# Performance work log

Measured on AMD Instinct MI355X. Metric: run time of the kernel, lower is better.

The kernel has to match this reference:

```python
import jax, jax.numpy as jnp
import numpy as np

D_IN = 768
D_OUT = 768
NUM_HEADS = 12
HEAD_DIM = D_OUT // NUM_HEADS


def setup_inputs() -> dict:
    key = jax.random.key(0)
    ks = jax.random.split(key, 6)
    s = 1.0 / np.sqrt(D_IN)
    X = jax.random.normal(ks[0], (4, 2048, D_IN), dtype=jnp.float32)
    Wq = jax.random.uniform(ks[1], (D_IN, D_OUT), jnp.float32, -s, s)
    Wk = jax.random.uniform(ks[2], (D_IN, D_OUT), jnp.float32, -s, s)
    Wv = jax.random.uniform(ks[3], (D_IN, D_OUT), jnp.float32, -s, s)
    Wo = jax.random.uniform(ks[4], (D_OUT, D_OUT), jnp.float32, -s, s)
    bo = jax.random.uniform(ks[5], (D_OUT,), jnp.float32, -s, s)
    return {"X": X, "Wq": Wq, "Wk": Wk, "Wv": Wv, "Wo": Wo, "bo": bo}


def reference(X, Wq, Wk, Wv, Wo, bo):
    b, n, _ = X.shape
    # QKV projections, split heads -> [b, h, n, d]
    def split(t):
        return t.reshape(b, n, NUM_HEADS, HEAD_DIM).transpose(0, 2, 1, 3)
    q = split(X @ Wq)
    k = split(X @ Wk)
    v = split(X @ Wv)
    scores = jnp.einsum('bhqd,bhkd->bhqk', q, k) / np.sqrt(HEAD_DIM).astype(np.float32)
    causal = jnp.triu(jnp.ones((n, n), dtype=bool), k=1)
    scores = jnp.where(causal, -jnp.inf, scores)
    attn = jax.nn.softmax(scores, axis=-1)  # dropout p=0 -> identity
    ctx = jnp.einsum('bhqk,bhkd->bhqd', attn, v)
    ctx = ctx.transpose(0, 2, 1, 3).reshape(b, n, D_OUT)
    return ctx @ Wo + bo
```

## Files before the change

kernel.cpp:

```cpp
#include <hip/hip_runtime.h>
#include <stdint.h>

#define B_  4
#define N_  2048
#define D_  768
#define H_  12
#define HD_ 64
#define M_  (B_*N_)

typedef short bf8 __attribute__((ext_vector_type(8)));
typedef float f32x4 __attribute__((ext_vector_type(4)));

static __device__ __forceinline__ unsigned short f2bf(float f) {
    unsigned u = __float_as_uint(f);
    unsigned r = u + 0x7fffu + ((u >> 16) & 1u);
    return (unsigned short)(r >> 16);
}

static __device__ __forceinline__ unsigned pk2bf(float f0, float f1) {
    return ((__float_as_uint(f1) + 0x8000u) & 0xFFFF0000u) |
           ((__float_as_uint(f0) + 0x8000u) >> 16);
}

#if __has_builtin(__builtin_amdgcn_exp2f)
#define EXP2(x) __builtin_amdgcn_exp2f(x)
#else
#define EXP2(x) exp2f(x)
#endif

#define GLOAD_LDS16(gptr, lptr)                                                   \
    __builtin_amdgcn_global_load_lds(                                             \
        (const __attribute__((address_space(1))) void*)(gptr),                    \
        (__attribute__((address_space(3))) void*)(lptr), 16, 0, 0)

#define QSCALE 0.1803368801111204f

__global__ __launch_bounds__(256) void convert_x(const float* __restrict__ X,
                                                 unsigned short* __restrict__ Xb) {
    const size_t i = ((size_t)blockIdx.x * 256 + threadIdx.x) * 8;
    const float4 a = *(const float4*)(X + i);
    const float4 b = *(const float4*)(X + i + 4);
    ushort4 lo, hi;
    lo.x = f2bf(a.x); lo.y = f2bf(a.y); lo.z = f2bf(a.z); lo.w = f2bf(a.w);
    hi.x = f2bf(b.x); hi.y = f2bf(b.y); hi.z = f2bf(b.z); hi.w = f2bf(b.w);
    *(ushort4*)(Xb + i)     = lo;
    *(ushort4*)(Xb + i + 4) = hi;
}

__global__ __launch_bounds__(256) void transpose_w(
    const float* __restrict__ Wq, const float* __restrict__ Wk,
    const float* __restrict__ Wv, const float* __restrict__ Wo,
    unsigned short* __restrict__ Wqt, unsigned short* __restrict__ Wkt,
    unsigned short* __restrict__ Wvt, unsigned short* __restrict__ Wot)
{
    __shared__ float tile[32][33];
    const int z = blockIdx.z;
    const float* W = (z == 0) ? Wq : (z == 1) ? Wk : (z == 2) ? Wv : Wo;
    unsigned short* Wt = (z == 0) ? Wqt : (z == 1) ? Wkt : (z == 2) ? Wvt : Wot;
    const int k0 = blockIdx.x * 32, n0 = blockIdx.y * 32;
    const int tx = threadIdx.x & 31, ty = threadIdx.x >> 5;
    #pragma unroll
    for (int i = 0; i < 4; ++i)
        tile[ty + 8 * i][tx] = W[(size_t)(k0 + ty + 8 * i) * D_ + n0 + tx];
    __syncthreads();
    #pragma unroll
    for (int i = 0; i < 4; ++i)
        Wt[(size_t)(n0 + ty + 8 * i) * D_ + k0 + tx] = f2bf(tile[tx][ty + 8 * i]);
}

__global__ __launch_bounds__(256) void qkv_mfma(
    const unsigned short* __restrict__ Xb,
    const unsigned short* __restrict__ Wqt, const unsigned short* __restrict__ Wkt,
    const unsigned short* __restrict__ Wvt,
    unsigned short* __restrict__ Qb, unsigned short* __restrict__ Kb,
    unsigned short* __restrict__ Vt)
{
    __shared__ unsigned short As[8192];
    __shared__ unsigned short Bs[8192];

    const int t = threadIdx.x;
    const int wave = t >> 6, lane = t & 63;
    const int col = lane & 15, quad = lane >> 4;
    const int wm = (wave & 1) * 64, wn = (wave >> 1) * 64;

    const int m0 = blockIdx.x * 128;
    const int n0 = blockIdx.y * 128;
    const int mat = blockIdx.z;
    const unsigned short* Wt = (mat == 0) ? Wqt : (mat == 1) ? Wkt : Wvt;
    const bool sw = (mat != 2);

    const unsigned short* Ag = Xb + (size_t)(m0 + (t >> 2)) * D_ + (t & 3) * 8;
    const unsigned short* Bg = Wt + (size_t)(n0 + (t >> 2)) * D_ + (t & 3) * 8;
    unsigned short* AsD = As + t * 8;
    unsigned short* BsD = Bs + t * 8;

    f32x4 acc[4][4] = {};

    for (int k0 = 0; k0 < D_; k0 += 64) {
        __syncthreads();
        GLOAD_LDS16(Ag + k0,                        AsD);
        GLOAD_LDS16(Ag + k0 + 32,                   AsD + 4096);
        GLOAD_LDS16(Ag + (size_t)64 * D_ + k0,      AsD + 2048);
        GLOAD_LDS16(Ag + (size_t)64 * D_ + k0 + 32, AsD + 6144);
        GLOAD_LDS16(Bg + k0,                        BsD);
        GLOAD_LDS16(Bg + k0 + 32,                   BsD + 4096);
        GLOAD_LDS16(Bg + (size_t)64 * D_ + k0,      BsD + 2048);
        GLOAD_LDS16(Bg + (size_t)64 * D_ + k0 + 32, BsD + 6144);
        __syncthreads();

        #pragma unroll
        for (int ks = 0; ks < 2; ++ks) {
            bf8 a[4], b[4];
            #pragma unroll
            for (int i = 0; i < 4; ++i)
                a[i] = *(const bf8*)(As + ks * 4096 + (wm + i * 16 + col) * 32 + quad * 8);
            #pragma unroll
            for (int j = 0; j < 4; ++j)
                b[j] = *(const bf8*)(Bs + ks * 4096 + (wn + j * 16 + col) * 32 + quad * 8);
            if (sw) {
                #pragma unroll
                for (int i = 0; i < 4; ++i)
                    #pragma unroll
                    for (int j = 0; j < 4; ++j)
                        acc[i][j] = __builtin_amdgcn_mfma_f32_16x16x32_bf16(b[j], a[i], acc[i][j], 0, 0, 0);
            } else {
                #pragma unroll
                for (int i = 0; i < 4; ++i)
                    #pragma unroll
                    for (int j = 0; j < 4; ++j)
                        acc[i][j] = __builtin_amdgcn_mfma_f32_16x16x32_bf16(a[i], b[j], acc[i][j], 0, 0, 0);
            }
        }
    }

    if (sw) {
        unsigned short* Out = (mat == 0) ? Qb : Kb;
        const float qsc = (mat == 0) ? QSCALE : 1.0f;
        #pragma unroll
        for (int i = 0; i < 4; ++i) {
            const int token = m0 + wm + i * 16 + col;
            const int bb = token >> 11, nn = token & (N_ - 1);
            #pragma unroll
            for (int j = 0; j < 4; ++j) {
                const int n = n0 + wn + j * 16 + quad * 4;
                const int h = n >> 6, d = n & 63;
                ushort4 pk;
                pk.x = f2bf(acc[i][j][0] * qsc);
                pk.y = f2bf(acc[i][j][1] * qsc);
                pk.z = f2bf(acc[i][j][2] * qsc);
                pk.w = f2bf(acc[i][j][3] * qsc);
                *(ushort4*)(Out + ((size_t)(bb * H_ + h) * N_ + nn) * HD_ + d) = pk;
            }
        }
    } else {
        #pragma unroll
        for (int j = 0; j < 4; ++j) {
            const int n = n0 + wn + j * 16 + col;
            const int h = n >> 6, d = n & 63;
            #pragma unroll
            for (int i = 0; i < 4; ++i) {
                const int mb = m0 + wm + i * 16 + quad * 4;
                const int bb = mb >> 11;
                const int nn = mb & (N_ - 1);
                const int nnp = (nn & ~31) | ((quad >> 1) << 4) | ((quad & 1) << 3) |
                                ((i & 1) << 2);
                ushort4 pk;
                pk.x = f2bf(acc[i][j][0]); pk.y = f2bf(acc[i][j][1]);
                pk.z = f2bf(acc[i][j][2]); pk.w = f2bf(acc[i][j][3]);
                *(ushort4*)(Vt + ((size_t)(bb * H_ + h) * HD_ + d) * N_ + nnp) = pk;
            }
        }
    }
}

#define PS 72

static __device__ __forceinline__ void qk_softmax(
    const bf8 (&ka)[4][2], bf8 qb0, bf8 qb1,
    int k0, int q, bool mask, float& lpart,
    bf8& pb0, bf8& pb1, int quad)
{
    f32x4 s[4] = {};
    __builtin_amdgcn_s_setprio(1);
    #pragma unroll
    for (int kc = 0; kc < 4; ++kc) {
        s[kc] = __builtin_amdgcn_mfma_f32_16x16x32_bf16(ka[kc][0], qb0, s[kc], 0, 0, 0);
        s[kc] = __builtin_amdgcn_mfma_f32_16x16x32_bf16(ka[kc][1], qb1, s[kc], 0, 0, 0);
    }
    __builtin_amdgcn_s_setprio(0);

    float p[4][4];
    if (mask) {
        #pragma unroll
        for (int kc = 0; kc < 4; ++kc)
            #pragma unroll
            for (int r = 0; r < 4; ++r) {
                const int key = k0 + kc * 16 + quad * 4 + r;
                p[kc][r] = EXP2((key > q) ? -INFINITY : s[kc][r]);
            }
    } else {
        #pragma unroll
        for (int kc = 0; kc < 4; ++kc)
            #pragma unroll
            for (int r = 0; r < 4; ++r) p[kc][r] = EXP2(s[kc][r]);
    }

    #pragma unroll
    for (int kc = 0; kc < 4; ++kc)
        #pragma unroll
        for (int r = 0; r < 4; ++r) lpart += p[kc][r];

    uint4 u0, u1;
    u0.x = pk2bf(p[0][0], p[0][1]); u0.y = pk2bf(p[0][2], p[0][3]);
    u0.z = pk2bf(p[1][0], p[1][1]); u0.w = pk2bf(p[1][2], p[1][3]);
    u1.x = pk2bf(p[2][0], p[2][1]); u1.y = pk2bf(p[2][2], p[2][3]);
    u1.z = pk2bf(p[3][0], p[3][1]); u1.w = pk2bf(p[3][2], p[3][3]);
    pb0 = *(bf8*)&u0;
    pb1 = *(bf8*)&u1;
}

static __device__ __forceinline__ void pv_acc(
    bf8 pb0, bf8 pb1, const bf8 (&va)[4][2], f32x4 (&o)[4])
{
    __builtin_amdgcn_s_setprio(1);
    #pragma unroll
    for (int dc = 0; dc < 4; ++dc) {
        o[dc] = __builtin_amdgcn_mfma_f32_16x16x32_bf16(va[dc][0], pb0, o[dc], 0, 0, 0);
        o[dc] = __builtin_amdgcn_mfma_f32_16x16x32_bf16(va[dc][1], pb1, o[dc], 0, 0, 0);
    }
    __builtin_amdgcn_s_setprio(0);
}

__global__ __launch_bounds__(256, 3) void attn_mfma(
    const unsigned short* __restrict__ Qb,
    const unsigned short* __restrict__ Kb,
    const unsigned short* __restrict__ Vt,
    unsigned short* __restrict__ Ctxb)
{
    __shared__ unsigned short Kl[2][64 * PS];
    __shared__ unsigned short Vl[2][64 * PS];

    const int t = threadIdx.x;
    const int wave = t >> 6;
    const int lane = t & 63;
    const int col  = lane & 15;
    const int quad = lane >> 4;

    const int bid = blockIdx.x;
    const int bh  = bid >> 4;
    const int x   = bid & 15;
    const int tl  = x, th = 31 - x;
    const int q0L = tl * 64 + wave * 16;
    const int q0H = th * 64 + wave * 16;
    const int qL  = q0L + col;
    const int qH  = q0H + col;

    const unsigned short* Kp = Kb + (size_t)bh * N_ * HD_;
    const unsigned short* Vp = Vt + (size_t)bh * HD_ * N_;
    const unsigned short* QpL = Qb + ((size_t)bh * N_ + q0L) * HD_;
    const unsigned short* QpH = Qb + ((size_t)bh * N_ + q0H) * HD_;

    const bf8 qbL0 = *(const bf8*)(QpL + (size_t)col * HD_ + quad * 8);
    const bf8 qbL1 = *(const bf8*)(QpL + (size_t)col * HD_ + 32 + quad * 8);
    const bf8 qbH0 = *(const bf8*)(QpH + (size_t)col * HD_ + quad * 8);
    const bf8 qbH1 = *(const bf8*)(QpH + (size_t)col * HD_ + 32 + quad * 8);

    f32x4 oL[4] = {}, oH[4] = {};
    float lL = 0.f, lH = 0.f;

    const int srow = t >> 3;
    const int scol = (t & 7) * 8;
    const unsigned short* Kg = Kp + (size_t)srow * HD_ + scol;
    const unsigned short* Vg = Vp + (size_t)srow * N_ + scol;
    const int kO0 = srow * PS + scol;
    const int kO1 = (srow + 32) * PS + scol;

    const int iters = 32 - x;

    uint4 kr0 = *(const uint4*)(Kg);
    uint4 kr1 = *(const uint4*)(Kg + (size_t)32 * HD_);
    uint4 vr0 = *(const uint4*)(Vg);
    uint4 vr1 = *(const uint4*)(Vg + (size_t)32 * N_);
    *(uint4*)(Kl[0] + kO0) = kr0;
    *(uint4*)(Kl[0] + kO1) = kr1;
    *(uint4*)(Vl[0] + kO0) = vr0;
    *(uint4*)(Vl[0] + kO1) = vr1;
    kr0 = *(const uint4*)(Kg + (size_t)64 * HD_);
    kr1 = *(const uint4*)(Kg + (size_t)96 * HD_);
    vr0 = *(const uint4*)(Vg + 64);
    vr1 = *(const uint4*)(Vg + (size_t)32 * N_ + 64);

    for (int kt = 0; kt < iters; ++kt) {
        const int k0 = kt * 64;
        const bool actL = (kt <= tl);
        const unsigned short* Kc = Kl[kt & 1];
        const unsigned short* Vc = Vl[kt & 1];
        unsigned short* Kn = Kl[(kt + 1) & 1];
        unsigned short* Vn = Vl[(kt + 1) & 1];

        __syncthreads();

        if (kt + 1 < iters) {
            *(uint4*)(Kn + kO0) = kr0;
            *(uint4*)(Kn + kO1) = kr1;
            *(uint4*)(Vn + kO0) = vr0;
            *(uint4*)(Vn + kO1) = vr1;
        }
        if (kt + 2 < iters) {
            const size_t k2 = (size_t)(kt + 2) * 64;
            kr0 = *(const uint4*)(Kg + k2 * HD_);
            kr1 = *(const uint4*)(Kg + (k2 + 32) * HD_);
            vr0 = *(const uint4*)(Vg + k2);
            vr1 = *(const uint4*)(Vg + (size_t)32 * N_ + k2);
        }

        bf8 ka[4][2];
        #pragma unroll
        for (int kc = 0; kc < 4; ++kc) {
            ka[kc][0] = *(const bf8*)(Kc + (kc * 16 + col) * PS + quad * 8);
            ka[kc][1] = *(const bf8*)(Kc + (kc * 16 + col) * PS + 32 + quad * 8);
        }

        bf8 va[4][2];
        #pragma unroll
        for (int dc = 0; dc < 4; ++dc) {
            va[dc][0] = *(const bf8*)(Vc + (dc * 16 + col) * PS + quad * 8);
            va[dc][1] = *(const bf8*)(Vc + (dc * 16 + col) * PS + 32 + quad * 8);
        }

        bf8 pbH0, pbH1;
        qk_softmax(ka, qbH0, qbH1, k0, qH, kt == th, lH, pbH0, pbH1, quad);
        pv_acc(pbH0, pbH1, va, oH);

        if (actL) {
            bf8 pbL0, pbL1;
            qk_softmax(ka, qbL0, qbL1, k0, qL, kt == tl, lL, pbL0, pbL1, quad);
            pv_acc(pbL0, pbL1, va, oL);
        }
    }

    const int b = bh / H_;
    const int h = bh % H_;
    {
        float l = lH;
        l += __shfl_xor(l, 16, 64);
        l += __shfl_xor(l, 32, 64);
        const float inv = 1.0f / l;
        unsigned short* cp = Ctxb + ((size_t)(b * N_ + qH)) * D_ + h * HD_;
        #pragma unroll
        for (int dc = 0; dc < 4; ++dc) {
            uint2 pk;
            pk.x = pk2bf(oH[dc][0] * inv, oH[dc][1] * inv);
            pk.y = pk2bf(oH[dc][2] * inv, oH[dc][3] * inv);
            *(uint2*)(cp + dc * 16 + quad * 4) = pk;
        }
    }
    {
        float l = lL;
        l += __shfl_xor(l, 16, 64);
        l += __shfl_xor(l, 32, 64);
        const float inv = 1.0f / l;
        unsigned short* cp = Ctxb + ((size_t)(b * N_ + qL)) * D_ + h * HD_;
        #pragma unroll
        for (int dc = 0; dc < 4; ++dc) {
            uint2 pk;
            pk.x = pk2bf(oL[dc][0] * inv, oL[dc][1] * inv);
            pk.y = pk2bf(oL[dc][2] * inv, oL[dc][3] * inv);
            *(uint2*)(cp + dc * 16 + quad * 4) = pk;
        }
    }
}

__global__ __launch_bounds__(256) void out_mfma(
    const unsigned short* __restrict__ Ctxb,
    const unsigned short* __restrict__ Wot,
    const float* __restrict__ bo,
    float* __restrict__ Out)
{
    __shared__ unsigned short As[8192];
    __shared__ unsigned short Bs[8192];

    const int t = threadIdx.x;
    const int wave = t >> 6, lane = t & 63;
    const int col = lane & 15, quad = lane >> 4;
    const int wm = (wave & 1) * 64, wn = (wave >> 1) * 64;

    const int m0 = blockIdx.x * 128;
    const int n0 = blockIdx.y * 128;

    const unsigned short* Ag = Ctxb + (size_t)(m0 + (t >> 2)) * D_ + (t & 3) * 8;
    const unsigned short* Bg = Wot + (size_t)(n0 + (t >> 2)) * D_ + (t & 3) * 8;
    unsigned short* AsD = As + t * 8;
    unsigned short* BsD = Bs + t * 8;

    f32x4 acc[4][4] = {};

    for (int k0 = 0; k0 < D_; k0 += 64) {
        __syncthreads();
        GLOAD_LDS16(Ag + k0,                        AsD);
        GLOAD_LDS16(Ag + k0 + 32,                   AsD + 4096);
        GLOAD_LDS16(Ag + (size_t)64 * D_ + k0,      AsD + 2048);
        GLOAD_LDS16(Ag + (size_t)64 * D_ + k0 + 32, AsD + 6144);
        GLOAD_LDS16(Bg + k0,                        BsD);
        GLOAD_LDS16(Bg + k0 + 32,                   BsD + 4096);
        GLOAD_LDS16(Bg + (size_t)64 * D_ + k0,      BsD + 2048);
        GLOAD_LDS16(Bg + (size_t)64 * D_ + k0 + 32, BsD + 6144);
        __syncthreads();

        #pragma unroll
        for (int ks = 0; ks < 2; ++ks) {
            bf8 a[4], b[4];
            #pragma unroll
            for (int i = 0; i < 4; ++i)
                a[i] = *(const bf8*)(As + ks * 4096 + (wm + i * 16 + col) * 32 + quad * 8);
            #pragma unroll
            for (int j = 0; j < 4; ++j)
                b[j] = *(const bf8*)(Bs + ks * 4096 + (wn + j * 16 + col) * 32 + quad * 8);
            #pragma unroll
            for (int i = 0; i < 4; ++i)
                #pragma unroll
                for (int j = 0; j < 4; ++j)
                    acc[i][j] = __builtin_amdgcn_mfma_f32_16x16x32_bf16(b[j], a[i], acc[i][j], 0, 0, 0);
        }
    }

    #pragma unroll
    for (int i = 0; i < 4; ++i) {
        const int m = m0 + wm + i * 16 + col;
        #pragma unroll
        for (int j = 0; j < 4; ++j) {
            const int n = n0 + wn + j * 16 + quad * 4;
            const float4 bias = *(const float4*)(bo + n);
            float4 o;
            o.x = acc[i][j][0] + bias.x;
            o.y = acc[i][j][1] + bias.y;
            o.z = acc[i][j][2] + bias.z;
            o.w = acc[i][j][3] + bias.w;
            *(float4*)(Out + (size_t)m * D_ + n) = o;
        }
    }
}

extern "C" void kernel_launch(void* const* d_in, const int* in_sizes, int n_in,
                              void* d_out, int out_size, void* d_ws, size_t ws_size,
                              hipStream_t stream) {
    const float* X  = (const float*)d_in[0];
    const float* Wq = (const float*)d_in[1];
    const float* Wk = (const float*)d_in[2];
    const float* Wv = (const float*)d_in[3];
    const float* Wo = (const float*)d_in[4];
    const float* bo = (const float*)d_in[5];
    float* out = (float*)d_out;

    const size_t elems = (size_t)M_ * D_;
    const size_t welems = (size_t)D_ * D_;
    unsigned short* Xb  = (unsigned short*)d_ws;
    unsigned short* Wqt = Xb + elems;
    unsigned short* Wkt = Wqt + welems;
    unsigned short* Wvt = Wkt + welems;
    unsigned short* Wot = Wvt + welems;
    unsigned short* Qb  = Wot + welems;
    unsigned short* Kb  = Qb + elems;
    unsigned short* Vt  = Kb + elems;
    unsigned short* Ctxb = Xb;

    convert_x<<<dim3(elems / 2048), 256, 0, stream>>>(X, Xb);
    transpose_w<<<dim3(24, 24, 4), 256, 0, stream>>>(Wq, Wk, Wv, Wo, Wqt, Wkt, Wvt, Wot);

    qkv_mfma<<<dim3(M_ / 128, D_ / 128, 3), 256, 0, stream>>>(Xb, Wqt, Wkt, Wvt, Qb, Kb, Vt);

    attn_mfma<<<dim3(B_ * H_ * 16), 256, 0, stream>>>(Qb, Kb, Vt, Ctxb);

    out_mfma<<<dim3(M_ / 128, D_ / 128), 256, 0, stream>>>(Ctxb, Wot, bo, out);
}
```

Before: 213.1 us.

## Remap block IDs for XCD-aware L2 locality and interleave QK MFMAs

Flattens the grids of the QKV and output GEMMs into 1D and remaps block IDs so that consecutive blocks on the same XCD (id mod 8) cover neighbouring tiles that share A and W data in L2. The attention kernel gets the same remap, so the 16 query-tile pairs of one head land on one XCD and reuse K/V. The attention loop also splits the QK MFMA step from the softmax and issues both the high and low QK MFMA groups before either softmax, which gives the scheduler more independent work to overlap. This costs more live registers (two score arrays), which could hurt occupancy at launch bounds of 3.

```diff
diff --git a/kernel.cpp b/kernel.cpp
--- a/kernel.cpp
+++ b/kernel.cpp
@@ -83,9 +83,12 @@
     const int col = lane & 15, quad = lane >> 4;
     const int wm = (wave & 1) * 64, wn = (wave >> 1) * 64;
 
-    const int m0 = blockIdx.x * 128;
-    const int n0 = blockIdx.y * 128;
-    const int mat = blockIdx.z;
+    const int orig = blockIdx.x;
+    const int wgid = (orig & 7) * 144 + (orig >> 3);
+    const int m0  = (wgid / 18) * 128;
+    const int nm  = wgid % 18;
+    const int mat = nm / 6;
+    const int n0  = (nm % 6) * 128;
     const unsigned short* Wt = (mat == 0) ? Wqt : (mat == 1) ? Wkt : Wvt;
     const bool sw = (mat != 2);
 
@@ -175,12 +178,9 @@
 
 #define PS 72
 
-static __device__ __forceinline__ void qk_softmax(
-    const bf8 (&ka)[4][2], bf8 qb0, bf8 qb1,
-    int k0, int q, bool mask, float& lpart,
-    bf8& pb0, bf8& pb1, int quad)
-{
-    f32x4 s[4] = {};
+static __device__ __forceinline__ void qk_mfma8(
+    const bf8 (&ka)[4][2], bf8 qb0, bf8 qb1, f32x4 (&s)[4])
+{
     __builtin_amdgcn_s_setprio(1);
     #pragma unroll
     for (int kc = 0; kc < 4; ++kc) {
@@ -188,7 +188,12 @@
         s[kc] = __builtin_amdgcn_mfma_f32_16x16x32_bf16(ka[kc][1], qb1, s[kc], 0, 0, 0);
     }
     __builtin_amdgcn_s_setprio(0);
-
+}
+
+static __device__ __forceinline__ void softmax_pack(
+    const f32x4 (&s)[4], int k0, int q, bool mask, float& lpart,
+    bf8& pb0, bf8& pb1, int quad)
+{
     float p[4][4];
     if (mask) {
         #pragma unroll
@@ -246,7 +251,8 @@
     const int col  = lane & 15;
     const int quad = lane >> 4;
 
-    const int bid = blockIdx.x;
+    const int orig = blockIdx.x;
+    const int bid  = (orig & 7) * 96 + (orig >> 3);
     const int bh  = bid >> 4;
     const int x   = bid & 15;
     const int tl  = x, th = 31 - x;
@@ -328,13 +334,18 @@
             va[dc][1] = *(const bf8*)(Vc + (dc * 16 + col) * PS + 32 + quad * 8);
         }
 
+        f32x4 sH[4] = {};
+        qk_mfma8(ka, qbH0, qbH1, sH);
+        f32x4 sL[4] = {};
+        if (actL) qk_mfma8(ka, qbL0, qbL1, sL);
+
         bf8 pbH0, pbH1;
-        qk_softmax(ka, qbH0, qbH1, k0, qH, kt == th, lH, pbH0, pbH1, quad);
+        softmax_pack(sH, k0, qH, kt == th, lH, pbH0, pbH1, quad);
         pv_acc(pbH0, pbH1, va, oH);
 
         if (actL) {
             bf8 pbL0, pbL1;
-            qk_softmax(ka, qbL0, qbL1, k0, qL, kt == tl, lL, pbL0, pbL1, quad);
+            softmax_pack(sL, k0, qL, kt == tl, lL, pbL0, pbL1, quad);
             pv_acc(pbL0, pbL1, va, oL);
         }
     }
@@ -385,8 +396,10 @@
     const int col = lane & 15, quad = lane >> 4;
     const int wm = (wave & 1) * 64, wn = (wave >> 1) * 64;
 
-    const int m0 = blockIdx.x * 128;
-    const int n0 = blockIdx.y * 128;
+    const int orig = blockIdx.x;
+    const int wgid = (orig & 7) * 48 + (orig >> 3);
+    const int m0 = (wgid / 6) * 128;
+    const int n0 = (wgid % 6) * 128;
 
     const unsigned short* Ag = Ctxb + (size_t)(m0 + (t >> 2)) * D_ + (t & 3) * 8;
     const unsigned short* Bg = Wot + (size_t)(n0 + (t >> 2)) * D_ + (t & 3) * 8;
@@ -467,9 +480,9 @@
     convert_x<<<dim3(elems / 2048), 256, 0, stream>>>(X, Xb);
     transpose_w<<<dim3(24, 24, 4), 256, 0, stream>>>(Wq, Wk, Wv, Wo, Wqt, Wkt, Wvt, Wot);
 
-    qkv_mfma<<<dim3(M_ / 128, D_ / 128, 3), 256, 0, stream>>>(Xb, Wqt, Wkt, Wvt, Qb, Kb, Vt);
+    qkv_mfma<<<dim3(1152), 256, 0, stream>>>(Xb, Wqt, Wkt, Wvt, Qb, Kb, Vt);
 
     attn_mfma<<<dim3(B_ * H_ * 16), 256, 0, stream>>>(Qb, Kb, Vt, Ctxb);
 
-    out_mfma<<<dim3(M_ / 128, D_ / 128), 256, 0, stream>>>(Ctxb, Wot, bo, out);
-}
+    out_mfma<<<dim3(384), 256, 0, stream>>>(Ctxb, Wot, bo, out);
+}
```

Measured after the change: 210.1 us. Within noise of the previous version (-1.4%).
